# Optimization experiments

Hardware: AMD Instinct MI355X
Metric: run time of the kernel (lower is better)

## Reference

```python
import jax, jax.numpy as jnp
import numpy as np

N_NODES = 50000
N_EDGES = 500000
IN_DIM = 256
HEADS = 4
OUT_C = 64
NEG_SLOPE = 0.2


def setup_inputs() -> dict:
    key = jax.random.key(0)
    ks = jax.random.split(key, 6)
    x = jax.random.normal(ks[0], (N_NODES, IN_DIM), dtype=jnp.float32)
    edge_index = jax.random.randint(ks[1], (2, N_EDGES), 0, N_NODES, dtype=jnp.int64)
    scale = 1.0 / np.sqrt(IN_DIM)
    W_l = jax.random.normal(ks[2], (IN_DIM, HEADS * OUT_C), dtype=jnp.float32) * scale
    W_r = jax.random.normal(ks[3], (IN_DIM, HEADS * OUT_C), dtype=jnp.float32) * scale
    b_l = jnp.zeros((HEADS * OUT_C,), dtype=jnp.float32)
    b_r = jnp.zeros((HEADS * OUT_C,), dtype=jnp.float32)
    att = jax.random.normal(ks[4], (HEADS, OUT_C), dtype=jnp.float32) * (1.0 / np.sqrt(OUT_C))
    bias = jnp.zeros((HEADS * OUT_C,), dtype=jnp.float32)
    return {"x": x, "edge_index": edge_index, "W_l": W_l, "b_l": b_l,
            "W_r": W_r, "b_r": b_r, "att": att, "bias": bias}


def _gatv2(x, edge_index, W_l, b_l, W_r, b_r, att, bias):
    N = x.shape[0]
    H, C = att.shape
    # add self loops (PyG GATv2Conv default add_self_loops=True)
    loop = jnp.arange(N, dtype=edge_index.dtype)
    src = jnp.concatenate([edge_index[0], loop])  # message sources (x_j)
    dst = jnp.concatenate([edge_index[1], loop])  # aggregation targets (x_i)
    x_l = (x @ W_l + b_l).reshape(N, H, C)  # source-side projection
    x_r = (x @ W_r + b_r).reshape(N, H, C)  # target-side projection
    # GATv2 attention logits: a^T LeakyReLU(x_l[src] + x_r[dst])
    e = jax.nn.leaky_relu(x_l[src] + x_r[dst], NEG_SLOPE)  # [E, H, C]
    logits = jnp.einsum('ehc,hc->eh', e, att)              # [E, H]
    # segmented softmax over incoming edges of each dst node
    m = jax.ops.segment_max(logits, dst, num_segments=N)   # [N, H]
    ex = jnp.exp(logits - m[dst])
    denom = jax.ops.segment_sum(ex, dst, num_segments=N)   # [N, H]
    alpha = ex / denom[dst]                                # [E, H]
    # weighted scatter-aggregation of source messages
    out = jax.ops.segment_sum(x_l[src] * alpha[:, :, None], dst, num_segments=N)  # [N, H, C]
    return out.reshape(N, H * C) + bias


def reference(x, edge_index, W_l, b_l, W_r, b_r, att, bias):
    out = _gatv2(x, edge_index, W_l, b_l, W_r, b_r, att, bias)  # [N, H*C]
    # wrapper: single relation -> reshape(-1, 1, output_dim) and cat on dim=1
    return out.reshape(-1, 1, HEADS * OUT_C)
```

## Files before the change

### kernel.cpp

```cpp
#include <hip/hip_runtime.h>
#include <hip/hip_bf16.h>
#include <math.h>

#define N_NODES 50000
#define N_PAD   50048
#define N_EDGES 500000
#define E_TOT   550000
#define HC      256
#define NHC     512
#define HEADS   4
#define NEG     0.2f

typedef __attribute__((ext_vector_type(8))) short short8;
typedef __attribute__((ext_vector_type(4))) float f32x4;
typedef __attribute__((ext_vector_type(2))) float f32x2;

__device__ __forceinline__ ushort f2bf(float f) {
    union { float f; unsigned u; } c; c.f = f;
    unsigned u = c.u;
    unsigned rounded = u + 0x7FFFu + ((u >> 16) & 1u);
    return (ushort)(rounded >> 16);
}

static constexpr size_t OFF_COUNTS = 0;
static constexpr size_t OFF_CUR    = OFF_COUNTS + (size_t)N_NODES * 4;
static constexpr size_t OFF_ROWS   = OFF_CUR + (size_t)N_NODES * 4;
static constexpr size_t OFF_SRCS   = OFF_ROWS + (size_t)(N_NODES + 1) * 4;
static constexpr size_t OFF_BSUM   = OFF_SRCS + (size_t)E_TOT * 4;
static constexpr size_t OFF_MODE   = OFF_BSUM + 64 * 4;
static constexpr size_t OFF_XB     = ((OFF_MODE + 4 + 255) / 256) * 256;
static constexpr size_t OFF_WT     = OFF_XB + (size_t)N_PAD * HC * 2;
static constexpr size_t OFF_XLB    = OFF_WT + (size_t)NHC * HC * 2;
static constexpr size_t OFF_XRB    = OFF_XLB + (size_t)N_NODES * HC * 2;

__device__ __forceinline__ int get_src(const int* __restrict__ ei, int mode, int e) {
    if (e >= N_EDGES) return e - N_EDGES;
    return mode ? ei[2 * e] : ei[e];
}
__device__ __forceinline__ int get_dst(const int* __restrict__ ei, int mode, int e) {
    if (e >= N_EDGES) return e - N_EDGES;
    return mode ? ei[2 * (N_EDGES + e)] : ei[N_EDGES + e];
}

#define XBLK 6256
#define WBLK 512
#define ZBLK 98
__global__ __launch_bounds__(256) void prep_kernel(
        const float* __restrict__ x, const float* __restrict__ Wl,
        const float* __restrict__ Wr, const int* __restrict__ ei,
        ushort* __restrict__ xb, ushort* __restrict__ wt,
        int* __restrict__ cz, int* __restrict__ mode) {
    const int b = blockIdx.x;
    if (b < XBLK) {
        size_t i = ((size_t)b * 256 + threadIdx.x) * 8;
        if (i >= (size_t)N_PAD * HC) return;
        ushort o[8];
        if (i < (size_t)N_NODES * HC) {
            float4 v0 = *(const float4*)(x + i);
            float4 v1 = *(const float4*)(x + i + 4);
            o[0] = f2bf(v0.x); o[1] = f2bf(v0.y); o[2] = f2bf(v0.z); o[3] = f2bf(v0.w);
            o[4] = f2bf(v1.x); o[5] = f2bf(v1.y); o[6] = f2bf(v1.z); o[7] = f2bf(v1.w);
        } else {
#pragma unroll
            for (int j = 0; j < 8; ++j) o[j] = 0;
        }
        *(short8*)(xb + i) = *(short8*)o;
    } else if (b < XBLK + WBLK) {
        int i = (b - XBLK) * 256 + threadIdx.x;
        int n = i >> 8, k = i & 255;
        float v = (n < HC) ? Wl[(size_t)k * HC + n] : Wr[(size_t)k * HC + (n - HC)];
        wt[i] = f2bf(v);
    } else if (b < XBLK + WBLK + ZBLK) {
        int i4 = (b - XBLK - WBLK) * 256 + threadIdx.x;
        if (i4 < 2 * N_NODES / 4) *(int4*)(cz + i4 * 4) = make_int4(0, 0, 0, 0);
    } else {
        __shared__ int any;
        if (threadIdx.x == 0) any = 0;
        __syncthreads();
        if (ei[2 * threadIdx.x + 1] != 0) atomicOr(&any, 1);
        __syncthreads();
        if (threadIdx.x == 0) mode[0] = (any == 0) ? 1 : 0;
    }
}

#define BM 128
#define BK 32
__global__ __launch_bounds__(256) void mfma_gemm_kernel(
        const __hip_bfloat16* __restrict__ xb, const __hip_bfloat16* __restrict__ wt,
        const float* __restrict__ bl, const float* __restrict__ br,
        ushort* __restrict__ xlb, ushort* __restrict__ xrb) {
    __shared__ ushort smem[4 * BM * BK];
    auto AS = [&](int buf) { return (__hip_bfloat16*)(smem + buf * BM * BK); };
    auto BS = [&](int buf) { return (__hip_bfloat16*)(smem + 2 * BM * BK + buf * BM * BK); };
    const int t    = threadIdx.x;
    const int lane = t & 63;
    const int wid  = t >> 6;
    const int wr   = wid >> 1, wc = wid & 1;
    const int brow = blockIdx.x * BM;
    const int bcol = blockIdx.y * BM;

    auto stage = [&](int buf, int k0) {
#pragma unroll
        for (int r = 0; r < 2; ++r) {
            int c = r * 256 + t;
            const __hip_bfloat16* ga = xb + ((size_t)(brow + (c >> 2)) * HC + k0 + (c & 3) * 8);
            __builtin_amdgcn_global_load_lds(
                (const __attribute__((address_space(1))) void*)ga,
                (__attribute__((address_space(3))) void*)((char*)AS(buf) + c * 16),
                16, 0, 0);
        }
#pragma unroll
        for (int r = 0; r < 2; ++r) {
            int c = r * 256 + t;
            const __hip_bfloat16* gb = wt + ((size_t)(bcol + (c >> 2)) * HC + k0 + (c & 3) * 8);
            __builtin_amdgcn_global_load_lds(
                (const __attribute__((address_space(1))) void*)gb,
                (__attribute__((address_space(3))) void*)((char*)BS(buf) + c * 16),
                16, 0, 0);
        }
    };

    f32x4 acc[4][4];
#pragma unroll
    for (int m = 0; m < 4; ++m)
#pragma unroll
        for (int n = 0; n < 4; ++n) acc[m][n] = (f32x4)0.f;

    stage(0, 0);
    __syncthreads();

    const int rsub = lane & 15;
    const int koff = (lane >> 4) * 16;

    for (int kk = 0; kk < 8; ++kk) {
        const int cur = kk & 1;
        if (kk < 7) stage(cur ^ 1, (kk + 1) * BK);
        short8 a[4], b[4];
#pragma unroll
        for (int m = 0; m < 4; ++m)
            a[m] = *(const short8*)((const char*)AS(cur) +
                    (wr * 64 + m * 16 + rsub) * (BK * 2) + koff);
#pragma unroll
        for (int n = 0; n < 4; ++n)
            b[n] = *(const short8*)((const char*)BS(cur) +
                    (wc * 64 + n * 16 + rsub) * (BK * 2) + koff);
#pragma unroll
        for (int m = 0; m < 4; ++m)
#pragma unroll
            for (int n = 0; n < 4; ++n)
                acc[m][n] = __builtin_amdgcn_mfma_f32_16x16x32_bf16(a[m], b[n], acc[m][n], 0, 0, 0);
        __syncthreads();
    }

    ushort* dst = (bcol < HC) ? xlb : xrb;
    const float* bvec = (bcol < HC) ? bl : br;
    const int cb = bcol & (HC - 1);
#pragma unroll
    for (int m = 0; m < 4; ++m) {
#pragma unroll
        for (int n = 0; n < 4; ++n) {
            int c_loc = wc * 64 + n * 16 + (lane & 15);
            float bv = bvec[cb + c_loc];
#pragma unroll
            for (int j = 0; j < 4; ++j) {
                int r_loc = wr * 64 + m * 16 + (lane >> 4) * 4 + j;
                smem[r_loc * 128 + (((c_loc >> 3) ^ (r_loc & 15)) * 8) + (c_loc & 7)] =
                    f2bf(acc[m][n][j] + bv);
            }
        }
    }
    __syncthreads();
    {
        const int r = t >> 1, hf = t & 1;
        if (brow + r < N_NODES) {
            ushort* gout = dst + (size_t)(brow + r) * HC + cb + hf * 64;
#pragma unroll
            for (int i = 0; i < 8; ++i) {
                int ci = hf * 8 + i;
                uint4 v = *(const uint4*)&smem[r * 128 + ((ci ^ (r & 15)) * 8)];
                *(uint4*)(gout + i * 8) = v;
            }
        }
    }
}

__global__ void count_kernel(const int* __restrict__ ei, const int* __restrict__ mode,
                             int* __restrict__ counts) {
    int e = blockIdx.x * blockDim.x + threadIdx.x;
    if (e < E_TOT) atomicAdd(&counts[get_dst(ei, *mode, e)], 1);
}

__global__ void scan1_kernel(const int* __restrict__ counts, int* __restrict__ rows,
                             int* __restrict__ bsum) {
    __shared__ int sdata[256];
    const int t = threadIdx.x;
    const int base = blockIdx.x * 1024 + t * 4;
    int v[4]; int s = 0;
#pragma unroll
    for (int j = 0; j < 4; ++j) {
        int idx = base + j;
        v[j] = (idx < N_NODES) ? counts[idx] : 0;
        s += v[j];
    }
    sdata[t] = s;
    __syncthreads();
    for (int off = 1; off < 256; off <<= 1) {
        int xv = (t >= off) ? sdata[t - off] : 0;
        __syncthreads();
        sdata[t] += xv;
        __syncthreads();
    }
    int run = sdata[t] - s;
#pragma unroll
    for (int j = 0; j < 4; ++j) {
        int idx = base + j;
        if (idx < N_NODES) rows[idx] = run;
        run += v[j];
    }
    if (t == 255) bsum[blockIdx.x] = sdata[255];
}

__global__ void scan2_kernel(int* __restrict__ bsum, int* __restrict__ rows) {
    if (threadIdx.x == 0 && blockIdx.x == 0) {
        int run = 0;
        for (int b = 0; b < 49; ++b) { int xv = bsum[b]; bsum[b] = run; run += xv; }
        rows[N_NODES] = E_TOT;
    }
}

__global__ void scan3_kernel(int* __restrict__ rows, const int* __restrict__ bsum) {
    int idx = blockIdx.x * 256 + threadIdx.x;
    if (idx < N_NODES) rows[idx] += bsum[idx >> 10];
}

__global__ void fill_kernel(const int* __restrict__ ei, const int* __restrict__ mode,
                            const int* __restrict__ rows, int* __restrict__ cursor,
                            int* __restrict__ srcs) {
    int e = blockIdx.x * blockDim.x + threadIdx.x;
    if (e < E_TOT) {
        int md = *mode;
        int d = get_dst(ei, md, e);
        int s = get_src(ei, md, e);
        int pos = atomicAdd(&cursor[d], 1);
        srcs[rows[d] + pos] = s;
    }
}

__global__ __launch_bounds__(256) void fused_agg_kernel(
        const ushort* __restrict__ xlb, const ushort* __restrict__ xrb,
        const float* __restrict__ att,
        const int* __restrict__ rows, const int* __restrict__ srcs,
        const float* __restrict__ bias, float* __restrict__ out) {
    const int lane = threadIdx.x & 63;
    const int n = (blockIdx.x * 256 + threadIdx.x) >> 6;
    if (n >= N_NODES) return;
    const int half = lane >> 5;
    const int sl   = lane & 31;
    const int start = rows[n], end = rows[n + 1];

    f32x2 xr2[4], at2[4];
    {
        uint4 c = *(const uint4*)(xrb + (size_t)n * HC + sl * 8);
        unsigned w[4] = {c.x, c.y, c.z, c.w};
#pragma unroll
        for (int j = 0; j < 4; ++j) {
            xr2[j][0] = __uint_as_float(w[j] << 16);
            xr2[j][1] = __uint_as_float(w[j] & 0xffff0000u);
        }
        float4 a0 = *(const float4*)&att[sl * 8];
        float4 a1 = *(const float4*)&att[sl * 8 + 4];
        at2[0][0] = a0.x; at2[0][1] = a0.y; at2[1][0] = a0.z; at2[1][1] = a0.w;
        at2[2][0] = a1.x; at2[2][1] = a1.y; at2[3][0] = a1.z; at2[3][1] = a1.w;
    }

    f32x2 acc2[4];
#pragma unroll
    for (int j = 0; j < 4; ++j) acc2[j] = (f32x2)0.f;
    float sm = 0.f;

    int i = start + half;
    uint4 rA = make_uint4(0, 0, 0, 0), rB = make_uint4(0, 0, 0, 0);
    int sC = -1;
    if (i < end)     rA = *(const uint4*)(xlb + (size_t)srcs[i] * HC + sl * 8);
    if (i + 2 < end) rB = *(const uint4*)(xlb + (size_t)srcs[i + 2] * HC + sl * 8);
    if (i + 4 < end) sC = srcs[i + 4];

    for (; i < end; i += 2) {
        uint4 r = rA;
        rA = rB;
        if (sC >= 0) rB = *(const uint4*)(xlb + (size_t)sC * HC + sl * 8);
        sC = (i + 6 < end) ? srcs[i + 6] : -1;

        unsigned w[4] = {r.x, r.y, r.z, r.w};
        f32x2 xv[4];
#pragma unroll
        for (int j = 0; j < 4; ++j) {
            xv[j][0] = __uint_as_float(w[j] << 16);
            xv[j][1] = __uint_as_float(w[j] & 0xffff0000u);
        }

        f32x2 p2 = (f32x2)0.f;
#pragma unroll
        for (int j = 0; j < 4; ++j) {
            f32x2 v = xv[j] + xr2[j];
            f32x2 lk = __builtin_elementwise_max(v, v * NEG);
            p2 = lk * at2[j] + p2;
        }
        float p = p2[0] + p2[1];
        p += __shfl_xor(p, 1, 64);
        p += __shfl_xor(p, 2, 64);
        p += __shfl_xor(p, 4, 64);

        float wgt = __expf(p);
        sm += wgt;
        f32x2 w2; w2[0] = wgt; w2[1] = wgt;
#pragma unroll
        for (int j = 0; j < 4; ++j) acc2[j] = xv[j] * w2 + acc2[j];
    }

    sm += __shfl_xor(sm, 32, 64);
#pragma unroll
    for (int j = 0; j < 4; ++j) {
        acc2[j][0] += __shfl_xor(acc2[j][0], 32, 64);
        acc2[j][1] += __shfl_xor(acc2[j][1], 32, 64);
    }

    if (half == 0) {
        const float inv = 1.0f / sm;
        float4 b0 = *(const float4*)&bias[sl * 8];
        float4 b1 = *(const float4*)&bias[sl * 8 + 4];
        float4 o0, o1;
        o0.x = fmaf(acc2[0][0], inv, b0.x); o0.y = fmaf(acc2[0][1], inv, b0.y);
        o0.z = fmaf(acc2[1][0], inv, b0.z); o0.w = fmaf(acc2[1][1], inv, b0.w);
        o1.x = fmaf(acc2[2][0], inv, b1.x); o1.y = fmaf(acc2[2][1], inv, b1.y);
        o1.z = fmaf(acc2[3][0], inv, b1.z); o1.w = fmaf(acc2[3][1], inv, b1.w);
        *(float4*)&out[(size_t)n * HC + sl * 8]     = o0;
        *(float4*)&out[(size_t)n * HC + sl * 8 + 4] = o1;
    }
}

extern "C" void kernel_launch(void* const* d_in, const int* in_sizes, int n_in,
                              void* d_out, int out_size, void* d_ws, size_t ws_size,
                              hipStream_t stream) {
    const float* x    = (const float*)d_in[0];
    const int*   ei   = (const int*)d_in[1];
    const float* Wl   = (const float*)d_in[2];
    const float* bl   = (const float*)d_in[3];
    const float* Wr   = (const float*)d_in[4];
    const float* br   = (const float*)d_in[5];
    const float* att  = (const float*)d_in[6];
    const float* bias = (const float*)d_in[7];
    float* out = (float*)d_out;

    char* ws = (char*)d_ws;
    int*   counts = (int*)(ws + OFF_COUNTS);
    int*   cursor = (int*)(ws + OFF_CUR);
    int*   rows   = (int*)(ws + OFF_ROWS);
    int*   srcs   = (int*)(ws + OFF_SRCS);
    int*   bsum   = (int*)(ws + OFF_BSUM);
    int*   mode   = (int*)(ws + OFF_MODE);
    ushort* xb    = (ushort*)(ws + OFF_XB);
    ushort* wt    = (ushort*)(ws + OFF_WT);
    ushort* xlb   = (ushort*)(ws + OFF_XLB);
    ushort* xrb   = (ushort*)(ws + OFF_XRB);

    prep_kernel<<<XBLK + WBLK + ZBLK + 1, 256, 0, stream>>>(
        x, Wl, Wr, ei, xb, wt, counts, mode);

    dim3 ggrid(N_PAD / BM, NHC / BM);
    mfma_gemm_kernel<<<ggrid, 256, 0, stream>>>(
        (const __hip_bfloat16*)xb, (const __hip_bfloat16*)wt, bl, br, xlb, xrb);

    count_kernel<<<(E_TOT + 255) / 256, 256, 0, stream>>>(ei, mode, counts);
    scan1_kernel<<<49, 256, 0, stream>>>(counts, rows, bsum);
    scan2_kernel<<<1, 64, 0, stream>>>(bsum, rows);
    scan3_kernel<<<(N_NODES + 255) / 256, 256, 0, stream>>>(rows, bsum);
    fill_kernel<<<(E_TOT + 255) / 256, 256, 0, stream>>>(ei, mode, rows, cursor, srcs);

    fused_agg_kernel<<<(N_NODES + 3) / 4, 256, 0, stream>>>(
        xlb, xrb, att, rows, srcs, bias, out);
}
```

Measured before the change: 166.2 us.

## Fuse edge counting into GEMM launch, fold block-sum scan into scan3

```diff
diff --git a/kernel.cpp b/kernel.cpp
--- a/kernel.cpp
+++ b/kernel.cpp
@@ -85,19 +85,31 @@
 
 #define BM 128
 #define BK 32
-__global__ __launch_bounds__(256) void mfma_gemm_kernel(
+#define GEMM_BLKS 1564
+#define CNT_BLKS  2149
+__global__ __launch_bounds__(256) void gemm_count_kernel(
         const __hip_bfloat16* __restrict__ xb, const __hip_bfloat16* __restrict__ wt,
         const float* __restrict__ bl, const float* __restrict__ br,
-        ushort* __restrict__ xlb, ushort* __restrict__ xrb) {
+        ushort* __restrict__ xlb, ushort* __restrict__ xrb,
+        const int* __restrict__ ei, const int* __restrict__ mode,
+        int* __restrict__ counts) {
     __shared__ ushort smem[4 * BM * BK];
+
+    if (blockIdx.x >= GEMM_BLKS) {
+        int e = (blockIdx.x - GEMM_BLKS) * 256 + threadIdx.x;
+        if (e < E_TOT) atomicAdd(&counts[get_dst(ei, *mode, e)], 1);
+        return;
+    }
+
     auto AS = [&](int buf) { return (__hip_bfloat16*)(smem + buf * BM * BK); };
     auto BS = [&](int buf) { return (__hip_bfloat16*)(smem + 2 * BM * BK + buf * BM * BK); };
     const int t    = threadIdx.x;
     const int lane = t & 63;
     const int wid  = t >> 6;
     const int wr   = wid >> 1, wc = wid & 1;
-    const int brow = blockIdx.x * BM;
-    const int bcol = blockIdx.y * BM;
+    const int bx   = blockIdx.x % 391, by = blockIdx.x / 391;
+    const int brow = bx * BM;
+    const int bcol = by * BM;
 
     auto stage = [&](int buf, int k0) {
 #pragma unroll
@@ -184,12 +196,6 @@
     }
 }
 
-__global__ void count_kernel(const int* __restrict__ ei, const int* __restrict__ mode,
-                             int* __restrict__ counts) {
-    int e = blockIdx.x * blockDim.x + threadIdx.x;
-    if (e < E_TOT) atomicAdd(&counts[get_dst(ei, *mode, e)], 1);
-}
-
 __global__ void scan1_kernel(const int* __restrict__ counts, int* __restrict__ rows,
                              int* __restrict__ bsum) {
     __shared__ int sdata[256];
@@ -220,17 +226,15 @@
     if (t == 255) bsum[blockIdx.x] = sdata[255];
 }
 
-__global__ void scan2_kernel(int* __restrict__ bsum, int* __restrict__ rows) {
-    if (threadIdx.x == 0 && blockIdx.x == 0) {
-        int run = 0;
-        for (int b = 0; b < 49; ++b) { int xv = bsum[b]; bsum[b] = run; run += xv; }
-        rows[N_NODES] = E_TOT;
-    }
-}
-
 __global__ void scan3_kernel(int* __restrict__ rows, const int* __restrict__ bsum) {
-    int idx = blockIdx.x * 256 + threadIdx.x;
-    if (idx < N_NODES) rows[idx] += bsum[idx >> 10];
+    const int idx = blockIdx.x * 256 + threadIdx.x;
+    const int r = blockIdx.x >> 2;
+    const int lane = threadIdx.x & 63;
+    int v = (lane < r) ? bsum[lane] : 0;
+#pragma unroll
+    for (int off = 1; off < 64; off <<= 1) v += __shfl_xor(v, off, 64);
+    if (idx < N_NODES) rows[idx] += v;
+    if (idx == 0) rows[N_NODES] = E_TOT;
 }
 
 __global__ void fill_kernel(const int* __restrict__ ei, const int* __restrict__ mode,
@@ -279,17 +283,15 @@
     float sm = 0.f;
 
     int i = start + half;
-    uint4 rA = make_uint4(0, 0, 0, 0), rB = make_uint4(0, 0, 0, 0);
-    int sC = -1;
-    if (i < end)     rA = *(const uint4*)(xlb + (size_t)srcs[i] * HC + sl * 8);
-    if (i + 2 < end) rB = *(const uint4*)(xlb + (size_t)srcs[i + 2] * HC + sl * 8);
-    if (i + 4 < end) sC = srcs[i + 4];
+    uint4 rA = make_uint4(0, 0, 0, 0);
+    int sB = -1;
+    if (i < end) rA = *(const uint4*)(xlb + (size_t)srcs[i] * HC + sl * 8);
+    if (i + 2 < end) sB = srcs[i + 2];
 
     for (; i < end; i += 2) {
         uint4 r = rA;
-        rA = rB;
-        if (sC >= 0) rB = *(const uint4*)(xlb + (size_t)sC * HC + sl * 8);
-        sC = (i + 6 < end) ? srcs[i + 6] : -1;
+        if (sB >= 0) rA = *(const uint4*)(xlb + (size_t)sB * HC + sl * 8);
+        sB = (i + 4 < end) ? srcs[i + 4] : -1;
 
         unsigned w[4] = {r.x, r.y, r.z, r.w};
         f32x2 xv[4];
@@ -367,14 +369,13 @@
     prep_kernel<<<XBLK + WBLK + ZBLK + 1, 256, 0, stream>>>(
         x, Wl, Wr, ei, xb, wt, counts, mode);
 
-    dim3 ggrid(N_PAD / BM, NHC / BM);
-    mfma_gemm_kernel<<<ggrid, 256, 0, stream>>>(
-        (const __hip_bfloat16*)xb, (const __hip_bfloat16*)wt, bl, br, xlb, xrb);
-
-    count_kernel<<<(E_TOT + 255) / 256, 256, 0, stream>>>(ei, mode, counts);
+    gemm_count_kernel<<<GEMM_BLKS + CNT_BLKS, 256, 0, stream>>>(
+        (const __hip_bfloat16*)xb, (const __hip_bfloat16*)wt, bl, br, xlb, xrb,
+        ei, mode, counts);
+
     scan1_kernel<<<49, 256, 0, stream>>>(counts, rows, bsum);
-    scan2_kernel<<<1, 64, 0, stream>>>(bsum, rows);
     scan3_kernel<<<(N_NODES + 255) / 256, 256, 0, stream>>>(rows, bsum);
+
     fill_kernel<<<(E_TOT + 255) / 256, 256, 0, stream>>>(ei, mode, rows, cursor, srcs);
 
     fused_agg_kernel<<<(N_NODES + 3) / 4, 256, 0, stream>>>(
```

Result: faster. 152.9 us (-8.0%).
